# Optimization experiments

Hardware: AMD Instinct MI355X
Metric: run time of the kernel (lower is better)

Reference implementation:

```python
import jax, jax.numpy as jnp
import numpy as np

HIDDEN = 1024
NUM_HEADS = 16
HEAD_DIM = 64
B, S = 2, 2048


def setup_inputs() -> dict:
    key = jax.random.key(0)
    k1, k2, k3 = jax.random.split(key, 3)
    x = jax.random.normal(k1, (B, S, HIDDEN), dtype=jnp.float32)
    # xavier-uniform style scaling for the projection weights
    lim_qkv = (6.0 / (HIDDEN + 3 * NUM_HEADS * HEAD_DIM)) ** 0.5
    lim_o = (6.0 / (NUM_HEADS * HEAD_DIM + HIDDEN)) ** 0.5
    w_qkv = jax.random.uniform(k2, (HIDDEN, 3 * NUM_HEADS * HEAD_DIM), jnp.float32, -lim_qkv, lim_qkv)
    w_o = jax.random.uniform(k3, (NUM_HEADS * HEAD_DIM, HIDDEN), jnp.float32, -lim_o, lim_o)
    return {"x": x, "w_qkv": w_qkv, "w_o": w_o}


def reference(x, w_qkv, w_o):
    b, s, _ = x.shape
    qkv = jnp.einsum('bsh,hf->bsf', x, w_qkv)               # [b, s, 3*H*D]
    qkv = qkv.reshape(b, s, 3, NUM_HEADS, HEAD_DIM)
    q = jnp.transpose(qkv[:, :, 0], (0, 2, 1, 3))           # [b, h, s, d]
    k = jnp.transpose(qkv[:, :, 1], (0, 2, 3, 1))           # [b, h, d, s]
    v = jnp.transpose(qkv[:, :, 2], (0, 2, 1, 3))           # [b, h, s, d]
    scores = jnp.einsum('bhqd,bhdk->bhqk', q, k) / jnp.sqrt(jnp.float32(HEAD_DIM))
    scores = jax.nn.softmax(scores, axis=-1)                # [b, h, q, k]
    # NOTE: faithful to source bug: sums over q, output indexed by k
    values = jnp.einsum('bhqk,bhkd->bhkd', scores, v)       # [b, h, s, d]
    values = jnp.transpose(values, (0, 2, 1, 3)).reshape(b, s, NUM_HEADS * HEAD_DIM)
    return jnp.einsum('bsf,fh->bsh', values, w_o)
```

## Files before the change

kernel.cpp:

```cpp
#include <hip/hip_runtime.h>
#include <stdint.h>


#define DEV static __device__ __forceinline__

typedef unsigned short u16;
typedef __attribute__((ext_vector_type(4))) float f32x4;
typedef __attribute__((ext_vector_type(16))) float f32x16;
typedef __bf16 bf16x8 __attribute__((ext_vector_type(8)));
typedef __attribute__((ext_vector_type(8))) unsigned short u16x8;
typedef __attribute__((ext_vector_type(4))) unsigned short u16x4;

#define QSCALE 0.18033688011112042f

DEV u16 f2bf(float f) {
    unsigned u = __builtin_bit_cast(unsigned, f);
    u += 0x7fffu + ((u >> 16) & 1u);
    return (u16)(u >> 16);
}
DEV float bf2f(u16 h) {
    unsigned u = ((unsigned)h) << 16;
    return __builtin_bit_cast(float, u);
}

DEV void async_copy16(const void* g, void* l) {
    __builtin_amdgcn_global_load_lds(
        (__attribute__((address_space(1))) void*)(g),
        (__attribute__((address_space(3))) void*)(l), 16, 0, 0);
}

#define WAITBAR_4 asm volatile("s_waitcnt vmcnt(4)\n\ts_barrier" ::: "memory")
#define WAITBAR_0 asm volatile("s_waitcnt vmcnt(0)\n\ts_barrier" ::: "memory")
#define BAR_ONLY  asm volatile("s_barrier" ::: "memory")

__global__ __launch_bounds__(256) void prep(
    const float* __restrict__ x, u16* __restrict__ xb,
    const float* __restrict__ wqkv, u16* __restrict__ wqkvT,
    const float* __restrict__ wo, u16* __restrict__ woT) {
    __shared__ float tile[32][33];
    const int bid = blockIdx.x;
    const int t = threadIdx.x;
    if (bid < 4096) {
        int i = bid * 256 + t;
        f32x4 v = *(const f32x4*)(x + (size_t)i * 4);
        u16x4 o;
#pragma unroll
        for (int j = 0; j < 4; j++) o[j] = f2bf(v[j]);
        *(u16x4*)(xb + (size_t)i * 4) = o;
        return;
    }
    const float* src;
    u16* dst;
    int rows, cols, c0, r0;
    if (bid < 7168) {
        int b2 = bid - 4096;
        src = wqkv; dst = wqkvT; rows = 1024; cols = 3072;
        c0 = (b2 % 96) * 32; r0 = (b2 / 96) * 32;
    } else {
        int b3 = bid - 7168;
        src = wo; dst = woT; rows = 1024; cols = 1024;
        c0 = (b3 % 32) * 32; r0 = (b3 / 32) * 32;
    }
    int tx = t & 31, ty = t >> 5;
#pragma unroll
    for (int i = 0; i < 4; i++)
        tile[ty + i * 8][tx] = src[(size_t)(r0 + ty + i * 8) * cols + c0 + tx];
    __syncthreads();
#pragma unroll
    for (int i = 0; i < 4; i++)
        dst[(size_t)(c0 + ty + i * 8) * rows + r0 + tx] = f2bf(tile[tx][ty + i * 8]);
}

__global__ __launch_bounds__(256) void gemm_qkv(
    const u16* __restrict__ A, const u16* __restrict__ Bt,
    u16* __restrict__ qb, u16* __restrict__ kb, u16* __restrict__ vb) {
    __shared__ __align__(16) u16 smem[128 * 136];
    const int t = threadIdx.x;
    const int wave = t >> 6;
    const int lane = t & 63;
    const int quad = lane >> 4;
    const int l16 = lane & 15;
    const int wr = wave >> 1;
    const int wc = wave & 1;
    const int bid = blockIdx.x;
    const int swz = (bid & 7) * 96 + (bid >> 3);
    const int n0 = (swz % 24) * 128;
    const int m0 = (swz / 24) * 128;

    f32x4 acc[4][4];
#pragma unroll
    for (int i = 0; i < 4; i++)
#pragma unroll
        for (int j = 0; j < 4; j++) acc[i][j] = {0.f, 0.f, 0.f, 0.f};

#define QKV_STAGE(buf, col)                                                     \
    {                                                                           \
        _Pragma("unroll") for (int i = 0; i < 2; i++) {                         \
            int idx = i * 256 + t;                                              \
            int row = idx >> 2, kc = idx & 3;                                   \
            int sb = kc ^ (row & 3);                                            \
            async_copy16(A + (size_t)(m0 + row) * 1024 + (col) + sb * 8,        \
                         &smem[(buf) * 8192 + idx * 8]);                        \
            async_copy16(Bt + (size_t)(n0 + row) * 1024 + (col) + sb * 8,       \
                         &smem[(buf) * 8192 + 4096 + idx * 8]);                 \
        }                                                                       \
    }

#define QKV_COMPUTE(buf)                                                        \
    {                                                                           \
        bf16x8 af[4], bfr[4];                                                   \
        _Pragma("unroll") for (int mt = 0; mt < 4; mt++) {                      \
            int row = wr * 64 + mt * 16 + l16;                                  \
            af[mt] = *(const bf16x8*)&smem[(buf) * 8192 + row * 32 +            \
                                           (quad ^ (row & 3)) * 8];             \
        }                                                                       \
        _Pragma("unroll") for (int nt = 0; nt < 4; nt++) {                      \
            int row = wc * 64 + nt * 16 + l16;                                  \
            bfr[nt] = *(const bf16x8*)&smem[(buf) * 8192 + 4096 + row * 32 +    \
                                            (quad ^ (row & 3)) * 8];            \
        }                                                                       \
        _Pragma("unroll") for (int mt = 0; mt < 4; mt++)                        \
            _Pragma("unroll") for (int nt = 0; nt < 4; nt++)                    \
                acc[mt][nt] = __builtin_amdgcn_mfma_f32_16x16x32_bf16(          \
                    af[mt], bfr[nt], acc[mt][nt], 0, 0, 0);                     \
    }

    QKV_STAGE(0, 0);
    for (int ks = 0; ks < 31; ks++) {
        const int cur = ks & 1;
        QKV_STAGE(cur ^ 1, (ks + 1) * 32);
        WAITBAR_4;
        QKV_COMPUTE(cur);
        BAR_ONLY;
    }
    WAITBAR_0;
    QKV_COMPUTE(1);
    BAR_ONLY;

    const int tsel = n0 >> 10;
    u16* dst = tsel == 0 ? qb : (tsel == 1 ? kb : vb);
    const float scl = tsel == 0 ? QSCALE : 1.0f;
#pragma unroll
    for (int mt = 0; mt < 4; mt++)
#pragma unroll
        for (int nt = 0; nt < 4; nt++) {
            int nn = wc * 64 + nt * 16 + l16;
#pragma unroll
            for (int r = 0; r < 4; r++) {
                int mm = wr * 64 + mt * 16 + quad * 4 + r;
                smem[mm * 136 + nn] = f2bf(acc[mt][nt][r] * scl);
            }
        }
    __syncthreads();
    const int col0 = (l16) * 8;
    const int rowb = (t >> 4);
    const int h0 = (n0 & 1023) >> 6;
#pragma unroll
    for (int i = 0; i < 8; i++) {
        int row = i * 16 + rowb;
        u16x8 v = *(const u16x8*)&smem[row * 136 + col0];
        int h = h0 + (col0 >> 6), d = col0 & 63;
        int mm = m0 + row;
        int b = mm >> 11, s = mm & 2047;
        *(u16x8*)&dst[((size_t)((b * 16 + h) * 2048 + s)) * 64 + d] = v;
    }
}

__global__ __launch_bounds__(256) void gemm_out(
    const u16* __restrict__ vb, const float* __restrict__ csum,
    const u16* __restrict__ Bt, float* __restrict__ out) {
    __shared__ __align__(16) u16 As[64 * 32];
    __shared__ __align__(16) u16 Bs[128 * 32];
    const int m0 = blockIdx.y * 64;
    const int n0 = blockIdx.x * 128;
    const int t = threadIdx.x;
    const int wave = t >> 6, lane = t & 63;
    const int quad = lane >> 4, l16 = lane & 15;
    const int wr = wave >> 1, wc = wave & 1;

    const int arow = m0 + (t >> 2);
    const int ab = arow >> 11, as = arow & 2047;

    f32x4 acc[2][4];
#pragma unroll
    for (int i = 0; i < 2; i++)
#pragma unroll
        for (int j = 0; j < 4; j++) acc[i][j] = {0.f, 0.f, 0.f, 0.f};

    for (int kt = 0; kt < 1024; kt += 32) {
        {
            int c = kt + (t & 3) * 8;
            int h = c >> 6, d0 = c & 63;
            int bh = ab * 16 + h;
            float cs = csum[bh * 2048 + as];
            u16x8 v = *(const u16x8*)&vb[((size_t)(bh * 2048 + as)) * 64 + d0];
            u16x8 o;
#pragma unroll
            for (int i = 0; i < 8; i++) o[i] = f2bf(bf2f(v[i]) * cs);
            *(u16x8*)&As[t * 8] = o;
        }
#pragma unroll
        for (int i = 0; i < 2; i++) {
            int idx = i * 256 + t;
            int row = idx >> 2, kc = idx & 3;
            async_copy16(Bt + (size_t)(n0 + row) * 1024 + kt + kc * 8, &Bs[idx * 8]);
        }
        __syncthreads();
        bf16x8 af[2], bfr[4];
#pragma unroll
        for (int mt = 0; mt < 2; mt++)
            af[mt] = *(const bf16x8*)&As[(wr * 32 + mt * 16 + l16) * 32 + quad * 8];
#pragma unroll
        for (int nt = 0; nt < 4; nt++)
            bfr[nt] = *(const bf16x8*)&Bs[(wc * 64 + nt * 16 + l16) * 32 + quad * 8];
#pragma unroll
        for (int mt = 0; mt < 2; mt++)
#pragma unroll
            for (int nt = 0; nt < 4; nt++)
                acc[mt][nt] = __builtin_amdgcn_mfma_f32_16x16x32_bf16(
                    af[mt], bfr[nt], acc[mt][nt], 0, 0, 0);
        __syncthreads();
    }
#pragma unroll
    for (int nt = 0; nt < 4; nt++) {
        int nn = n0 + wc * 64 + nt * 16 + l16;
#pragma unroll
        for (int mt = 0; mt < 2; mt++) {
#pragma unroll
            for (int r = 0; r < 4; r++) {
                int mm = m0 + wr * 32 + mt * 16 + quad * 4 + r;
                out[(size_t)mm * 1024 + nn] = acc[mt][nt][r];
            }
        }
    }
}


__global__ __launch_bounds__(256) void attn_pass1(
    const u16* __restrict__ qb, const u16* __restrict__ kb,
    float* __restrict__ lp, float* __restrict__ csum) {
    __shared__ __align__(16) u16 Ks[2][128 * 64];
    const int t = threadIdx.x;
    const int wave = t >> 6;
    const int lane = t & 63;
    const int l32 = lane & 31, half = lane >> 5;
    const int kchunk = blockIdx.x & 3;
    const int qblk = (blockIdx.x >> 2) & 7;
    const int bh = blockIdx.x >> 5;
    const int q0 = qblk * 256 + wave * 64;

    if (blockIdx.x < 256) csum[blockIdx.x * 256 + t] = 0.f;

    bf16x8 a[2][4];
#pragma unroll
    for (int qs = 0; qs < 2; qs++) {
        const u16* Qr = qb + (size_t)(bh * 2048 + q0 + qs * 32 + l32) * 64 + half * 8;
#pragma unroll
        for (int f = 0; f < 4; f++) a[qs][f] = *(const bf16x8*)&Qr[f * 16];
    }

    const u16* Kbase = kb + (size_t)(bh * 2048 + kchunk * 512) * 64;

    float lsum[2][16];
#pragma unroll
    for (int qs = 0; qs < 2; qs++)
#pragma unroll
        for (int r = 0; r < 16; r++) lsum[qs][r] = 0.f;

    f32x16 ZZ;
#pragma unroll
    for (int r = 0; r < 16; r++) ZZ[r] = 0.f;

#define STAGE_K(buf, kt)                                                        \
    {                                                                           \
        _Pragma("unroll") for (int i = 0; i < 4; i++) {                         \
            int idx = i * 256 + t;                                              \
            int row = idx >> 3;                                                 \
            int blk = (idx & 7) ^ (row & 7);                                    \
            async_copy16(Kbase + (size_t)((kt) * 128 + row) * 64 + blk * 8,     \
                         &Ks[buf][idx * 8]);                                    \
        }                                                                       \
    }

#define COMPUTE_K(cur)                                                          \
    {                                                                           \
        _Pragma("unroll") for (int sub = 0; sub < 4; sub++) {                   \
            const int row = sub * 32 + l32;                                     \
            const int r7 = row & 7;                                             \
            bf16x8 bfr[4];                                                      \
            _Pragma("unroll") for (int f = 0; f < 4; f++)                       \
                bfr[f] = *(const bf16x8*)&Ks[cur][row * 64 +                    \
                                                 (((f * 2 + half)) ^ r7) * 8];  \
            __builtin_amdgcn_s_setprio(1);                                      \
            _Pragma("unroll") for (int qs = 0; qs < 2; qs++) {                  \
                f32x16 acc = __builtin_amdgcn_mfma_f32_32x32x16_bf16(           \
                    a[qs][0], bfr[0], ZZ, 0, 0, 0);                             \
                _Pragma("unroll") for (int f = 1; f < 4; f++)                   \
                    acc = __builtin_amdgcn_mfma_f32_32x32x16_bf16(              \
                        a[qs][f], bfr[f], acc, 0, 0, 0);                        \
                __builtin_amdgcn_s_setprio(0);                                  \
                _Pragma("unroll") for (int r = 0; r < 16; r++)                  \
                    lsum[qs][r] += __builtin_amdgcn_exp2f(acc[r]);              \
                __builtin_amdgcn_s_setprio(1);                                  \
            }                                                                   \
            __builtin_amdgcn_s_setprio(0);                                     \
        }                                                                       \
    }

    STAGE_K(0, 0);
    for (int kt = 0; kt < 3; kt++) {
        const int cur = kt & 1;
        STAGE_K(cur ^ 1, kt + 1);
        WAITBAR_4;
        COMPUTE_K(cur);
        BAR_ONLY;
    }
    WAITBAR_0;
    COMPUTE_K(1);

#pragma unroll
    for (int qs = 0; qs < 2; qs++) {
#pragma unroll
        for (int r = 0; r < 16; r++) {
            float v = lsum[qs][r];
            v += __shfl_xor(v, 1);
            v += __shfl_xor(v, 2);
            v += __shfl_xor(v, 4);
            v += __shfl_xor(v, 8);
            v += __shfl_xor(v, 16);
            lsum[qs][r] = v;
        }
    }
    if (l32 == 0) {
#pragma unroll
        for (int qs = 0; qs < 2; qs++) {
            float* dst = lp + kchunk * 65536 + bh * 2048 + q0 + qs * 32 + half * 4;
#pragma unroll
            for (int r = 0; r < 16; r++)
                dst[(r & 3) + 8 * (r >> 2)] = lsum[qs][r];
        }
    }
}

__global__ __launch_bounds__(256) void attn_pass2(
    const u16* __restrict__ qb, const u16* __restrict__ kb,
    const float* __restrict__ lp, float* __restrict__ csum) {
    __shared__ __align__(16) u16 Qs[2][128 * 64];
    __shared__ __align__(16) float li_lds[512];
    const int t = threadIdx.x;
    const int wave = t >> 6;
    const int lane = t & 63;
    const int l32 = lane & 31, half = lane >> 5;
    const int qchunk = blockIdx.x & 3;
    const int kblk = (blockIdx.x >> 2) & 7;
    const int bh = blockIdx.x >> 5;
    const int k0 = kblk * 256 + wave * 64;

    {
        const int base = bh * 2048 + qchunk * 512;
#pragma unroll
        for (int i = 0; i < 2; i++) {
            int q = i * 256 + t;
            float s = lp[base + q] + lp[65536 + base + q] + lp[131072 + base + q] +
                      lp[196608 + base + q];
            li_lds[q] = 1.0f / s;
        }
    }

    bf16x8 b[2][4];
#pragma unroll
    for (int ks = 0; ks < 2; ks++) {
        const u16* Kr = kb + (size_t)(bh * 2048 + k0 + ks * 32 + l32) * 64 + half * 8;
#pragma unroll
        for (int f = 0; f < 4; f++) b[ks][f] = *(const bf16x8*)&Kr[f * 16];
    }

    const u16* Qbase = qb + (size_t)(bh * 2048 + qchunk * 512) * 64;

    f32x16 ZZ;
#pragma unroll
    for (int r = 0; r < 16; r++) ZZ[r] = 0.f;

#define STAGE_Q(buf, qt)                                                        \
    {                                                                           \
        _Pragma("unroll") for (int i = 0; i < 4; i++) {                         \
            int idx = i * 256 + t;                                              \
            int row = idx >> 3;                                                 \
            int blk = (idx & 7) ^ (row & 7);                                    \
            async_copy16(Qbase + (size_t)((qt) * 128 + row) * 64 + blk * 8,     \
                         &Qs[buf][idx * 8]);                                    \
        }                                                                       \
    }

#define COMPUTE_Q(cur, qt)                                                      \
    {                                                                           \
        _Pragma("unroll") for (int sub = 0; sub < 4; sub++) {                   \
            const int row = sub * 32 + l32;                                     \
            const int r7 = row & 7;                                             \
            bf16x8 af[4];                                                       \
            _Pragma("unroll") for (int f = 0; f < 4; f++)                       \
                af[f] = *(const bf16x8*)&Qs[cur][row * 64 +                     \
                                                 (((f * 2 + half)) ^ r7) * 8];  \
            const float* lr = &li_lds[(qt) * 128 + sub * 32 + half * 4];        \
            f32x4 li0 = *(const f32x4*)&lr[0];                                  \
            f32x4 li1 = *(const f32x4*)&lr[8];                                  \
            f32x4 li2 = *(const f32x4*)&lr[16];                                 \
            f32x4 li3 = *(const f32x4*)&lr[24];                                 \
            __builtin_amdgcn_s_setprio(1);                                      \
            _Pragma("unroll") for (int ks = 0; ks < 2; ks++) {                  \
                f32x16 acc = __builtin_amdgcn_mfma_f32_32x32x16_bf16(           \
                    af[0], b[ks][0], ZZ, 0, 0, 0);                              \
                _Pragma("unroll") for (int f = 1; f < 4; f++)                   \
                    acc = __builtin_amdgcn_mfma_f32_32x32x16_bf16(              \
                        af[f], b[ks][f], acc, 0, 0, 0);                         \
                __builtin_amdgcn_s_setprio(0);                                  \
                float c = cs[ks];                                               \
                _Pragma("unroll") for (int r = 0; r < 4; r++)                   \
                    c += __builtin_amdgcn_exp2f(acc[r]) * li0[r];               \
                _Pragma("unroll") for (int r = 0; r < 4; r++)                   \
                    c += __builtin_amdgcn_exp2f(acc[4 + r]) * li1[r];           \
                _Pragma("unroll") for (int r = 0; r < 4; r++)                   \
                    c += __builtin_amdgcn_exp2f(acc[8 + r]) * li2[r];           \
                _Pragma("unroll") for (int r = 0; r < 4; r++)                   \
                    c += __builtin_amdgcn_exp2f(acc[12 + r]) * li3[r];          \
                cs[ks] = c;                                                     \
                __builtin_amdgcn_s_setprio(1);                                  \
            }                                                                   \
            __builtin_amdgcn_s_setprio(0);                                     \
        }                                                                       \
    }

    float cs[2] = {0.f, 0.f};
    __syncthreads();
    STAGE_Q(0, 0);

    for (int qt = 0; qt < 3; qt++) {
        const int cur = qt & 1;
        STAGE_Q(cur ^ 1, qt + 1);
        WAITBAR_4;
        COMPUTE_Q(cur, qt);
        BAR_ONLY;
    }
    WAITBAR_0;
    COMPUTE_Q(1, 3);

#pragma unroll
    for (int ks = 0; ks < 2; ks++) {
        float v = cs[ks] + __shfl_xor(cs[ks], 32);
        if (lane < 32)
            atomicAdd(&csum[bh * 2048 + k0 + ks * 32 + lane], v);
    }
}


extern "C" void kernel_launch(void* const* d_in, const int* in_sizes, int n_in,
                              void* d_out, int out_size, void* d_ws, size_t ws_size,
                              hipStream_t stream) {
    const float* x    = (const float*)d_in[0];
    const float* wqkv = (const float*)d_in[1];
    const float* wo   = (const float*)d_in[2];
    float* out = (float*)d_out;
    char* ws = (char*)d_ws;

    u16* xb      = (u16*)(ws);
    u16* wqkvT   = (u16*)(ws + 8388608);
    u16* woT     = (u16*)(ws + 14680064);
    u16* qb      = (u16*)(ws + 16777216);
    u16* kb      = (u16*)(ws + 25165824);
    u16* vb      = (u16*)(ws + 33554432);
    float* lp    = (float*)(ws);
    float* csum  = (float*)(ws + 42467328);

    prep<<<8192, 256, 0, stream>>>(x, xb, wqkv, wqkvT, wo, woT);
    gemm_qkv<<<768, 256, 0, stream>>>(xb, wqkvT, qb, kb, vb);
    attn_pass1<<<1024, 256, 0, stream>>>(qb, kb, lp, csum);
    attn_pass2<<<1024, 256, 0, stream>>>(qb, kb, lp, csum);
    gemm_out<<<dim3(8, 64), 256, 0, stream>>>(vb, csum, woT, out);
}
```

Before: 200.7 us.

## Give each wave private LDS double buffers to drop block barriers in attention passes

```diff
diff --git a/kernel.cpp b/kernel.cpp
--- a/kernel.cpp
+++ b/kernel.cpp
@@ -32,6 +32,9 @@
 #define WAITBAR_4 asm volatile("s_waitcnt vmcnt(4)\n\ts_barrier" ::: "memory")
 #define WAITBAR_0 asm volatile("s_waitcnt vmcnt(0)\n\ts_barrier" ::: "memory")
 #define BAR_ONLY  asm volatile("s_barrier" ::: "memory")
+#define WAIT_LG0 asm volatile("s_waitcnt lgkmcnt(0)" ::: "memory")
+#define WAIT_VM4 asm volatile("s_waitcnt vmcnt(4)" ::: "memory")
+#define WAIT_VM0 asm volatile("s_waitcnt vmcnt(0)" ::: "memory")
 
 __global__ __launch_bounds__(256) void prep(
     const float* __restrict__ x, u16* __restrict__ xb,
@@ -239,7 +242,7 @@
 __global__ __launch_bounds__(256) void attn_pass1(
     const u16* __restrict__ qb, const u16* __restrict__ kb,
     float* __restrict__ lp, float* __restrict__ csum) {
-    __shared__ __align__(16) u16 Ks[2][128 * 64];
+    __shared__ __align__(16) u16 Ks[4][2][32 * 64];
     const int t = threadIdx.x;
     const int wave = t >> 6;
     const int lane = t & 63;
@@ -260,6 +263,8 @@
     }
 
     const u16* Kbase = kb + (size_t)(bh * 2048 + kchunk * 512) * 64;
+    u16* KsW = &Ks[wave][0][0];
+    const int srow = lane >> 3, sslot = lane & 7;
 
     float lsum[2][16];
 #pragma unroll
@@ -271,52 +276,48 @@
 #pragma unroll
     for (int r = 0; r < 16; r++) ZZ[r] = 0.f;
 
-#define STAGE_K(buf, kt)                                                        \
+#define STAGE_W1(buf, tt)                                                       \
     {                                                                           \
         _Pragma("unroll") for (int i = 0; i < 4; i++) {                         \
-            int idx = i * 256 + t;                                              \
-            int row = idx >> 3;                                                 \
-            int blk = (idx & 7) ^ (row & 7);                                    \
-            async_copy16(Kbase + (size_t)((kt) * 128 + row) * 64 + blk * 8,     \
-                         &Ks[buf][idx * 8]);                                    \
-        }                                                                       \
-    }
-
-#define COMPUTE_K(cur)                                                          \
-    {                                                                           \
-        _Pragma("unroll") for (int sub = 0; sub < 4; sub++) {                   \
-            const int row = sub * 32 + l32;                                     \
-            const int r7 = row & 7;                                             \
-            bf16x8 bfr[4];                                                      \
-            _Pragma("unroll") for (int f = 0; f < 4; f++)                       \
-                bfr[f] = *(const bf16x8*)&Ks[cur][row * 64 +                    \
-                                                 (((f * 2 + half)) ^ r7) * 8];  \
+            int row = i * 8 + srow;                                             \
+            int blk = sslot ^ (row & 7);                                        \
+            async_copy16(Kbase + (size_t)((tt) * 32 + row) * 64 + blk * 8,      \
+                         &KsW[(buf) * 2048 + i * 512]);                         \
+        }                                                                       \
+    }
+
+#define COMPUTE_W1(buf)                                                         \
+    {                                                                           \
+        const int r7 = l32 & 7;                                                 \
+        bf16x8 bfr[4];                                                          \
+        _Pragma("unroll") for (int f = 0; f < 4; f++)                           \
+            bfr[f] = *(const bf16x8*)&KsW[(buf) * 2048 + l32 * 64 +             \
+                                          ((f * 2 + half) ^ r7) * 8];           \
+        __builtin_amdgcn_s_setprio(1);                                          \
+        _Pragma("unroll") for (int qs = 0; qs < 2; qs++) {                      \
+            f32x16 acc = __builtin_amdgcn_mfma_f32_32x32x16_bf16(               \
+                a[qs][0], bfr[0], ZZ, 0, 0, 0);                                 \
+            _Pragma("unroll") for (int f = 1; f < 4; f++)                       \
+                acc = __builtin_amdgcn_mfma_f32_32x32x16_bf16(                  \
+                    a[qs][f], bfr[f], acc, 0, 0, 0);                            \
+            __builtin_amdgcn_s_setprio(0);                                      \
+            _Pragma("unroll") for (int r = 0; r < 16; r++)                      \
+                lsum[qs][r] += __builtin_amdgcn_exp2f(acc[r]);                  \
             __builtin_amdgcn_s_setprio(1);                                      \
-            _Pragma("unroll") for (int qs = 0; qs < 2; qs++) {                  \
-                f32x16 acc = __builtin_amdgcn_mfma_f32_32x32x16_bf16(           \
-                    a[qs][0], bfr[0], ZZ, 0, 0, 0);                             \
-                _Pragma("unroll") for (int f = 1; f < 4; f++)                   \
-                    acc = __builtin_amdgcn_mfma_f32_32x32x16_bf16(              \
-                        a[qs][f], bfr[f], acc, 0, 0, 0);                        \
-                __builtin_amdgcn_s_setprio(0);                                  \
-                _Pragma("unroll") for (int r = 0; r < 16; r++)                  \
-                    lsum[qs][r] += __builtin_amdgcn_exp2f(acc[r]);              \
-                __builtin_amdgcn_s_setprio(1);                                  \
-            }                                                                   \
-            __builtin_amdgcn_s_setprio(0);                                     \
-        }                                                                       \
-    }
-
-    STAGE_K(0, 0);
-    for (int kt = 0; kt < 3; kt++) {
-        const int cur = kt & 1;
-        STAGE_K(cur ^ 1, kt + 1);
-        WAITBAR_4;
-        COMPUTE_K(cur);
-        BAR_ONLY;
-    }
-    WAITBAR_0;
-    COMPUTE_K(1);
+        }                                                                       \
+        __builtin_amdgcn_s_setprio(0);                                          \
+    }
+
+    STAGE_W1(0, 0);
+    for (int tt = 0; tt < 15; tt++) {
+        const int cur = tt & 1;
+        WAIT_LG0;
+        STAGE_W1(cur ^ 1, tt + 1);
+        WAIT_VM4;
+        COMPUTE_W1(cur);
+    }
+    WAIT_VM0;
+    COMPUTE_W1(1);
 
 #pragma unroll
     for (int qs = 0; qs < 2; qs++) {
@@ -345,7 +346,7 @@
 __global__ __launch_bounds__(256) void attn_pass2(
     const u16* __restrict__ qb, const u16* __restrict__ kb,
     const float* __restrict__ lp, float* __restrict__ csum) {
-    __shared__ __align__(16) u16 Qs[2][128 * 64];
+    __shared__ __align__(16) u16 Qs[4][2][32 * 64];
     __shared__ __align__(16) float li_lds[512];
     const int t = threadIdx.x;
     const int wave = t >> 6;
@@ -376,73 +377,71 @@
     }
 
     const u16* Qbase = qb + (size_t)(bh * 2048 + qchunk * 512) * 64;
+    u16* QsW = &Qs[wave][0][0];
+    const int srow = lane >> 3, sslot = lane & 7;
 
     f32x16 ZZ;
 #pragma unroll
     for (int r = 0; r < 16; r++) ZZ[r] = 0.f;
 
-#define STAGE_Q(buf, qt)                                                        \
+#define STAGE_W2(buf, tt)                                                       \
     {                                                                           \
         _Pragma("unroll") for (int i = 0; i < 4; i++) {                         \
-            int idx = i * 256 + t;                                              \
-            int row = idx >> 3;                                                 \
-            int blk = (idx & 7) ^ (row & 7);                                    \
-            async_copy16(Qbase + (size_t)((qt) * 128 + row) * 64 + blk * 8,     \
-                         &Qs[buf][idx * 8]);                                    \
-        }                                                                       \
-    }
-
-#define COMPUTE_Q(cur, qt)                                                      \
-    {                                                                           \
-        _Pragma("unroll") for (int sub = 0; sub < 4; sub++) {                   \
-            const int row = sub * 32 + l32;                                     \
-            const int r7 = row & 7;                                             \
-            bf16x8 af[4];                                                       \
-            _Pragma("unroll") for (int f = 0; f < 4; f++)                       \
-                af[f] = *(const bf16x8*)&Qs[cur][row * 64 +                     \
-                                                 (((f * 2 + half)) ^ r7) * 8];  \
-            const float* lr = &li_lds[(qt) * 128 + sub * 32 + half * 4];        \
-            f32x4 li0 = *(const f32x4*)&lr[0];                                  \
-            f32x4 li1 = *(const f32x4*)&lr[8];                                  \
-            f32x4 li2 = *(const f32x4*)&lr[16];                                 \
-            f32x4 li3 = *(const f32x4*)&lr[24];                                 \
+            int row = i * 8 + srow;                                             \
+            int blk = sslot ^ (row & 7);                                        \
+            async_copy16(Qbase + (size_t)((tt) * 32 + row) * 64 + blk * 8,      \
+                         &QsW[(buf) * 2048 + i * 512]);                         \
+        }                                                                       \
+    }
+
+#define COMPUTE_W2(buf, tt)                                                     \
+    {                                                                           \
+        const int r7 = l32 & 7;                                                 \
+        bf16x8 af[4];                                                           \
+        _Pragma("unroll") for (int f = 0; f < 4; f++)                           \
+            af[f] = *(const bf16x8*)&QsW[(buf) * 2048 + l32 * 64 +              \
+                                         ((f * 2 + half) ^ r7) * 8];            \
+        const float* lr = &li_lds[(tt) * 32 + half * 4];                        \
+        f32x4 li0 = *(const f32x4*)&lr[0];                                      \
+        f32x4 li1 = *(const f32x4*)&lr[8];                                      \
+        f32x4 li2 = *(const f32x4*)&lr[16];                                     \
+        f32x4 li3 = *(const f32x4*)&lr[24];                                     \
+        __builtin_amdgcn_s_setprio(1);                                          \
+        _Pragma("unroll") for (int ks = 0; ks < 2; ks++) {                      \
+            f32x16 acc = __builtin_amdgcn_mfma_f32_32x32x16_bf16(               \
+                af[0], b[ks][0], ZZ, 0, 0, 0);                                  \
+            _Pragma("unroll") for (int f = 1; f < 4; f++)                       \
+                acc = __builtin_amdgcn_mfma_f32_32x32x16_bf16(                  \
+                    af[f], b[ks][f], acc, 0, 0, 0);                             \
+            __builtin_amdgcn_s_setprio(0);                                      \
+            float c = cs[ks];                                                   \
+            _Pragma("unroll") for (int r = 0; r < 4; r++)                       \
+                c += __builtin_amdgcn_exp2f(acc[r]) * li0[r];                   \
+            _Pragma("unroll") for (int r = 0; r < 4; r++)                       \
+                c += __builtin_amdgcn_exp2f(acc[4 + r]) * li1[r];               \
+            _Pragma("unroll") for (int r = 0; r < 4; r++)                       \
+                c += __builtin_amdgcn_exp2f(acc[8 + r]) * li2[r];               \
+            _Pragma("unroll") for (int r = 0; r < 4; r++)                       \
+                c += __builtin_amdgcn_exp2f(acc[12 + r]) * li3[r];              \
+            cs[ks] = c;                                                         \
             __builtin_amdgcn_s_setprio(1);                                      \
-            _Pragma("unroll") for (int ks = 0; ks < 2; ks++) {                  \
-                f32x16 acc = __builtin_amdgcn_mfma_f32_32x32x16_bf16(           \
-                    af[0], b[ks][0], ZZ, 0, 0, 0);                              \
-                _Pragma("unroll") for (int f = 1; f < 4; f++)                   \
-                    acc = __builtin_amdgcn_mfma_f32_32x32x16_bf16(              \
-                        af[f], b[ks][f], acc, 0, 0, 0);                         \
-                __builtin_amdgcn_s_setprio(0);                                  \
-                float c = cs[ks];                                               \
-                _Pragma("unroll") for (int r = 0; r < 4; r++)                   \
-                    c += __builtin_amdgcn_exp2f(acc[r]) * li0[r];               \
-                _Pragma("unroll") for (int r = 0; r < 4; r++)                   \
-                    c += __builtin_amdgcn_exp2f(acc[4 + r]) * li1[r];           \
-                _Pragma("unroll") for (int r = 0; r < 4; r++)                   \
-                    c += __builtin_amdgcn_exp2f(acc[8 + r]) * li2[r];           \
-                _Pragma("unroll") for (int r = 0; r < 4; r++)                   \
-                    c += __builtin_amdgcn_exp2f(acc[12 + r]) * li3[r];          \
-                cs[ks] = c;                                                     \
-                __builtin_amdgcn_s_setprio(1);                                  \
-            }                                                                   \
-            __builtin_amdgcn_s_setprio(0);                                     \
-        }                                                                       \
+        }                                                                       \
+        __builtin_amdgcn_s_setprio(0);                                          \
     }
 
     float cs[2] = {0.f, 0.f};
     __syncthreads();
-    STAGE_Q(0, 0);
-
-    for (int qt = 0; qt < 3; qt++) {
-        const int cur = qt & 1;
-        STAGE_Q(cur ^ 1, qt + 1);
-        WAITBAR_4;
-        COMPUTE_Q(cur, qt);
-        BAR_ONLY;
-    }
-    WAITBAR_0;
-    COMPUTE_Q(1, 3);
+    STAGE_W2(0, 0);
+
+    for (int tt = 0; tt < 15; tt++) {
+        const int cur = tt & 1;
+        WAIT_LG0;
+        STAGE_W2(cur ^ 1, tt + 1);
+        WAIT_VM4;
+        COMPUTE_W2(cur, tt);
+    }
+    WAIT_VM0;
+    COMPUTE_W2(1, 15);
 
 #pragma unroll
     for (int ks = 0; ks < 2; ks++) {
```

Measured after the change: 206.3 us. 1.03x slower.
